# Performance work log

Measured on AMD Instinct MI355X. Metric: run time of the kernel, lower is better.

## Reference

```python
import jax, jax.numpy as jnp
import numpy as np

NUM_HEADS = 8
TOP_M = 128


def setup_inputs() -> dict:
    key = jax.random.key(0)
    ks = jax.random.split(key, 4)
    B, N, C = 2, 4096, 512
    x = jax.random.normal(ks[0], (B, N, C), dtype=jnp.float32)
    # nn.Linear-style params (stored as [in, out] for x @ W)
    qkv_w = jax.random.normal(ks[1], (C, 3 * C), dtype=jnp.float32) * (C ** -0.5)
    qkv_b = jnp.zeros((3 * C,), dtype=jnp.float32)
    proj_w = jax.random.normal(ks[2], (C, C), dtype=jnp.float32) * (C ** -0.5)
    proj_b = jnp.zeros((C,), dtype=jnp.float32)
    return {"x": x, "qkv_w": qkv_w, "qkv_b": qkv_b, "proj_w": proj_w, "proj_b": proj_b}


def reference(x, qkv_w, qkv_b, proj_w, proj_b):
    B, N, C = x.shape
    H = NUM_HEADS
    hd = C // H
    scale = hd ** -0.5

    qkv = x @ qkv_w + qkv_b                       # [B, N, 3C]
    qkv = qkv.reshape(B, N, 3, H, hd).transpose(2, 0, 3, 1, 4)  # [3, B, H, N, hd]
    q, k, v = qkv[0], qkv[1], qkv[2]

    attn = jnp.einsum("bhnd,bhmd->bhnm", q, k) * scale  # [B, H, N, N]

    if TOP_M < N:
        _, topk_idx = jax.lax.top_k(attn, TOP_M)         # [B, H, N, m]
        keep = jnp.put_along_axis(
            jnp.zeros(attn.shape, dtype=bool), topk_idx, True, axis=-1, inplace=False
        )
        attn = jnp.where(keep, attn, -jnp.inf)

    p = jax.nn.softmax(attn, axis=-1)                    # dropout is identity (p=0)
    out = jnp.einsum("bhnm,bhmd->bhnd", p, v)            # [B, H, N, hd]
    out = out.transpose(0, 2, 1, 3).reshape(B, N, C)
    return out @ proj_w + proj_b
```

## Files before the change

kernel.cpp:

```cpp
#include <hip/hip_runtime.h>
#include <cstdint>
#include <cstddef>


typedef float f32x4 __attribute__((ext_vector_type(4)));
typedef __bf16 bf16x8 __attribute__((ext_vector_type(8)));
typedef __bf16 bf16x4 __attribute__((ext_vector_type(4)));

#define MFMA16(a, b, c) __builtin_amdgcn_mfma_f32_16x16x32_bf16((a), (b), (c), 0, 0, 0)

static __device__ __forceinline__ void async_ld16(const void* g, void* l) {
  __builtin_amdgcn_global_load_lds(
      (const __attribute__((address_space(1))) unsigned int*)g,
      (__attribute__((address_space(3))) unsigned int*)l, 16, 0, 0);
}

static __device__ __forceinline__ float bf16raw_to_f32(unsigned r) {
  return __uint_as_float(r << 16);
}

__global__ void k_split(const float* __restrict__ src, __bf16* __restrict__ dh,
                        __bf16* __restrict__ dl, int n) {
  const int i = (blockIdx.x * 256 + threadIdx.x) * 4;
  if (i >= n) return;
  const float4 v = *(const float4*)(src + i);
  bf16x4 h, l;
  h[0] = (__bf16)v.x; l[0] = (__bf16)(v.x - (float)h[0]);
  h[1] = (__bf16)v.y; l[1] = (__bf16)(v.y - (float)h[1]);
  h[2] = (__bf16)v.z; l[2] = (__bf16)(v.z - (float)h[2]);
  h[3] = (__bf16)v.w; l[3] = (__bf16)(v.w - (float)h[3]);
  *(bf16x4*)(dh + i) = h;
  *(bf16x4*)(dl + i) = l;
}

__global__ void k_splitT(const float* __restrict__ src, __bf16* __restrict__ dh,
                         __bf16* __restrict__ dl, int N) {
  const int idx = blockIdx.x * 256 + threadIdx.x;
  const int k = idx & 511;
  const int n = idx >> 9;
  if (n >= N) return;
  const float v = src[(size_t)k * N + n];
  const __bf16 hi = (__bf16)v;
  dh[idx] = hi;
  dl[idx] = (__bf16)(v - (float)hi);
}

template <int MODE>
__global__ __launch_bounds__(256, 2) void k_gemm(
    const __bf16* __restrict__ Agh, const __bf16* __restrict__ Agl,
    const __bf16* __restrict__ Bgh, const __bf16* __restrict__ Bgl,
    const float* __restrict__ bias, float* __restrict__ Cout,
    __bf16* __restrict__ qh, __bf16* __restrict__ ql,
    __bf16* __restrict__ kf,
    __bf16* __restrict__ vv, int N, int K) {
  __shared__ __bf16 sAh[4096], sAl[4096], sBh[4096], sBl[4096];

  const int tid = threadIdx.x;
  const int lane = tid & 63;
  const int wave = tid >> 6;
  const int wm = wave >> 1, wn = wave & 1;
  const int row0 = blockIdx.x * 128;
  const int col0 = blockIdx.y * 128;
  const int m15 = lane & 15, q4 = lane >> 4;

  f32x4 acc[4][4] = {};

  for (int k0 = 0; k0 < K; k0 += 32) {
    __syncthreads();
#pragma unroll
    for (int c = 0; c < 2; ++c) {
      const int s = c * 4 + wave;
      const int gr = s * 16 + m15;
      const int gk = k0 + q4 * 8;
      const size_t aoff = (size_t)(row0 + gr) * K + gk;
      const size_t boff = (size_t)(col0 + gr) * K + gk;
      const int lb = s * 512;
      async_ld16(Agh + aoff, sAh + lb);
      async_ld16(Agl + aoff, sAl + lb);
      async_ld16(Bgh + boff, sBh + lb);
      async_ld16(Bgl + boff, sBl + lb);
    }
    __syncthreads();

    bf16x8 afh[4], afl[4];
#pragma unroll
    for (int mt = 0; mt < 4; ++mt) {
      const int o = (wm * 4 + mt) * 512 + lane * 8;
      afh[mt] = *(const bf16x8*)(sAh + o);
      afl[mt] = *(const bf16x8*)(sAl + o);
    }
#pragma unroll
    for (int nt = 0; nt < 4; ++nt) {
      const int o = (wn * 4 + nt) * 512 + lane * 8;
      const bf16x8 bfh = *(const bf16x8*)(sBh + o);
      const bf16x8 bfl = *(const bf16x8*)(sBl + o);
#pragma unroll
      for (int mt = 0; mt < 4; ++mt) {
        acc[mt][nt] = MFMA16(afh[mt], bfh, acc[mt][nt]);
        acc[mt][nt] = MFMA16(afh[mt], bfl, acc[mt][nt]);
        acc[mt][nt] = MFMA16(afl[mt], bfh, acc[mt][nt]);
      }
    }
  }

#pragma unroll
  for (int mt = 0; mt < 4; ++mt) {
#pragma unroll
    for (int nt = 0; nt < 4; ++nt) {
      const int col = col0 + wn * 64 + nt * 16 + m15;
      const float bcol = bias[col];
#pragma unroll
      for (int r = 0; r < 4; ++r) {
        const int row = row0 + wm * 64 + mt * 16 + q4 * 4 + r;
        const float val = acc[mt][nt][r] + bcol;
        if (MODE == 1) {
          Cout[(size_t)row * N + col] = val;
        } else {
          const int t = col >> 9;
          const int cc = col & 511;
          const int h = cc >> 6, d = cc & 63;
          const int b = row >> 12, n = row & 4095;
          const int bh2 = b * 8 + h;
          if (t == 2) {
            vv[((size_t)bh2 * 4096 + n) * 64 + d] = (__bf16)val;
          } else if (t == 0) {
            const float sv = val * 0.125f;
            const __bf16 hi = (__bf16)sv;
            const size_t o = ((size_t)bh2 * 4096 + n) * 64 + d;
            qh[o] = hi;
            ql[o] = (__bf16)(sv - (float)hi);
          } else {
            const int tt = n >> 4, m = n & 15;
            const int half = d >> 5, q4e = (d & 31) >> 3, e = d & 7;
            const size_t o = ((size_t)(bh2 * 256 + tt) * 4 + half) * 512 +
                             (q4e * 16 + m) * 8 + e;
            const __bf16 hi = (__bf16)val;
            kf[o] = hi;
            kf[o + 1024] = (__bf16)(val - (float)hi);
          }
        }
      }
    }
  }
}

#define CAP 432
#define NBINS 128
__global__ __launch_bounds__(1024, 8) void k_attn(
    const __bf16* __restrict__ qh, const __bf16* __restrict__ ql,
    const __bf16* __restrict__ kf,
    const __bf16* __restrict__ vv, __bf16* __restrict__ ah,
    __bf16* __restrict__ al) {
  __shared__ unsigned int cand[32][CAP];
  __shared__ unsigned int hist[16][NBINS];
  __shared__ unsigned int blist[16][48];
  __shared__ float rsum[32], rsum2[32], t0s[32], invq[32], dqs[32], mrefs[32];
  __shared__ unsigned int ccnt[32];
  __shared__ unsigned int bcnt[16];

  const int tid = threadIdx.x;
  const int lane = tid & 63;
  const int wave = tid >> 6;
  const int m15 = lane & 15, q4 = lane >> 4;
  const int rt = wave & 1;
  const int cr = wave >> 1;
  const int cbase = cr * 512;

  const int L = blockIdx.x;
  const int s = L >> 3;
  const int bh = (L & 7) * 2 + (s >> 7);
  const int row0 = (s & 127) * 32;
  const size_t base = (size_t)bh * 4096 * 64;

  if (tid < 32) { rsum[tid] = 0.f; rsum2[tid] = 0.f; ccnt[tid] = 0; }
  __syncthreads();

  bf16x8 qfh[2], qfl[2];
  {
    const size_t qo = base + (size_t)(row0 + rt * 16 + m15) * 64 + q4 * 8;
    qfh[0] = *(const bf16x8*)(qh + qo);
    qfl[0] = *(const bf16x8*)(ql + qo);
    qfh[1] = *(const bf16x8*)(qh + qo + 32);
    qfl[1] = *(const bf16x8*)(ql + qo + 32);
  }
  const __bf16* kt_base = kf + ((size_t)(bh * 256 + cr * 32) * 4) * 512;
  const int l8 = lane * 8;

  {
    float s1[4] = {0.f, 0.f, 0.f, 0.f}, s2[4] = {0.f, 0.f, 0.f, 0.f};
    for (int j = 0; j < 8; ++j) {
      const __bf16* kt = kt_base + (size_t)(j * 4) * 2048;
      const bf16x8 ch0 = *(const bf16x8*)(kt + l8);
      const bf16x8 ch1 = *(const bf16x8*)(kt + 512 + l8);
      const bf16x8 cl0 = *(const bf16x8*)(kt + 1024 + l8);
      const bf16x8 cl1 = *(const bf16x8*)(kt + 1536 + l8);
      f32x4 a = {0.f, 0.f, 0.f, 0.f};
      a = MFMA16(qfh[0], ch0, a);
      a = MFMA16(qfh[1], ch1, a);
      a = MFMA16(qfh[0], cl0, a);
      a = MFMA16(qfh[1], cl1, a);
      a = MFMA16(qfl[0], ch0, a);
      a = MFMA16(qfl[1], ch1, a);
#pragma unroll
      for (int r = 0; r < 4; ++r) { s1[r] += a[r]; s2[r] += a[r] * a[r]; }
    }
#pragma unroll
    for (int o = 1; o < 16; o <<= 1)
#pragma unroll
      for (int r = 0; r < 4; ++r) {
        s1[r] += __shfl_xor(s1[r], o);
        s2[r] += __shfl_xor(s2[r], o);
      }
    if (m15 == 0) {
#pragma unroll
      for (int r = 0; r < 4; ++r) {
        atomicAdd(&rsum[rt * 16 + q4 * 4 + r], s1[r]);
        atomicAdd(&rsum2[rt * 16 + q4 * 4 + r], s2[r]);
      }
    }
  }
  __syncthreads();
  if (tid < 32) {
    const float mu = rsum[tid] * (1.f / 1024.f);
    float var = rsum2[tid] * (1.f / 1024.f) - mu * mu;
    const float sd = sqrtf(fmaxf(var, 1e-12f));
    t0s[tid] = mu + 1.45f * sd;
    invq[tid] = 1048575.0f / (8.0f * sd);
    dqs[tid]  = (8.0f * sd) * (1.0f / 1048576.0f);
    mrefs[tid] = mu + 5.0f * sd;
  }
  __syncthreads();

  float t0r[4], ivr[4];
#pragma unroll
  for (int r = 0; r < 4; ++r) {
    t0r[r] = t0s[rt * 16 + q4 * 4 + r];
    ivr[r] = invq[rt * 16 + q4 * 4 + r];
  }

  for (int t = 0; t < 32; ++t) {
    const __bf16* kt = kt_base + (size_t)t * 2048;
    const bf16x8 ch0 = *(const bf16x8*)(kt + l8);
    const bf16x8 ch1 = *(const bf16x8*)(kt + 512 + l8);
    const bf16x8 cl0 = *(const bf16x8*)(kt + 1024 + l8);
    const bf16x8 cl1 = *(const bf16x8*)(kt + 1536 + l8);
    f32x4 a = {0.f, 0.f, 0.f, 0.f};
    a = MFMA16(qfh[0], ch0, a);
    a = MFMA16(qfh[1], ch1, a);
    a = MFMA16(qfh[0], cl0, a);
    a = MFMA16(qfh[1], cl1, a);
    a = MFMA16(qfl[0], ch0, a);
    a = MFMA16(qfl[1], ch1, a);
    const unsigned col = (unsigned)(cbase + t * 16 + m15);
#pragma unroll
    for (int r = 0; r < 4; ++r) {
      const float sc = a[r];
      if (sc > t0r[r]) {
        const int row = rt * 16 + q4 * 4 + r;
        int qv = (int)((sc - t0r[r]) * ivr[r]);
        qv = qv > 0xFFFFF ? 0xFFFFF : qv;
        const unsigned e = ((unsigned)qv << 12) | col;
        const unsigned idx = atomicAdd(&ccnt[row], 1u);
        if (idx < CAP) cand[row][idx] = e;
      }
    }
  }
  __syncthreads();

  const unsigned long long bel = (1ull << lane) - 1ull;
  for (int j = 0; j < 2; ++j) {
    const int row = wave * 2 + j;
    const unsigned cnt = min(ccnt[row], (unsigned)CAP);
    const float t0 = t0s[row], dq = dqs[row], mref = mrefs[row];

    hist[wave][lane] = 0;
    hist[wave][lane + 64] = 0;
    if (lane == 0) bcnt[wave] = 0;
    for (unsigned i = lane; i < cnt; i += 64)
      atomicAdd(&hist[wave][cand[row][i] >> 25], 1u);

    const unsigned h0 = hist[wave][2 * lane];
    const unsigned h1 = hist[wave][2 * lane + 1];
    unsigned S = h0 + h1;
    for (int o = 1; o < 64; o <<= 1) {
      const unsigned tmp = __shfl_down(S, o);
      if (lane + o < 64) S += tmp;
    }
    unsigned Snext = __shfl_down(S, 1);
    if (lane == 63) Snext = 0;
    const bool owner = (S >= 128u) && (Snext < 128u);
    const unsigned long long msk = __ballot(owner);
    unsigned thrE = 0;
    if (msk != 0ull) {
      const int ol = __ffsll((unsigned long long)msk) - 1;
      int Bv = 0;
      unsigned rv = 128;
      if (owner) {
        if (Snext + h1 >= 128u) { Bv = 2 * lane + 1; rv = 128u - Snext; }
        else { Bv = 2 * lane; rv = 128u - (Snext + h1); }
      }
      const int B = __shfl(Bv, ol);
      const unsigned rneed = (unsigned)__shfl((int)rv, ol);
      for (unsigned i = lane; i < cnt; i += 64) {
        const unsigned e = cand[row][i];
        if ((int)(e >> 25) == B) {
          const unsigned u = atomicAdd(&bcnt[wave], 1u);
          if (u < 48) blist[wave][u] = e;
        }
      }
      const unsigned ml = min(bcnt[wave], 48u);
      const unsigned mye = (lane < (int)ml) ? blist[wave][lane] : 0u;
      unsigned rlt = 0;
      for (unsigned jj = 0; jj < ml; ++jj)
        rlt += (blist[wave][jj] > mye) ? 1u : 0u;
      const bool hit = (lane < (int)ml) && (rlt == rneed - 1u);
      const unsigned long long hm = __ballot(hit);
      if (hm != 0ull) thrE = __shfl(mye, __ffsll((unsigned long long)hm) - 1);
    }

    unsigned outc = 0;
    float zpart = 0.f;
    for (unsigned c = 0; c * 64 < cnt; ++c) {
      const unsigned i = c * 64 + lane;
      bool sl = false;
      unsigned e = 0;
      if (i < cnt) { e = cand[row][i]; sl = (e >= thrE); }
      const unsigned long long mb = __ballot(sl);
      if (sl) {
        const unsigned pos = outc + (unsigned)__popcll(mb & bel);
        const float scr = t0 + (float)(e >> 12) * dq;
        const float p = __expf(scr - mref);
        zpart += p;
        cand[row][pos] = (__float_as_uint(p) & 0xFFFFF000u) | (e & 0xFFFu);
      }
      outc += (unsigned)__popcll(mb);
    }
#pragma unroll
    for (int o = 1; o < 64; o <<= 1) zpart += __shfl_xor(zpart, o);
    const int n = (int)outc;

    {
      const char* vb2 = (const char*)(vv + base) + lane * 2;
      float o8[8] = {0.f, 0.f, 0.f, 0.f, 0.f, 0.f, 0.f, 0.f};
      int i = 0;
      for (; i + 8 <= n; i += 8) {
        unsigned e0 = cand[row][i + 0], e1 = cand[row][i + 1];
        unsigned e2 = cand[row][i + 2], e3 = cand[row][i + 3];
        unsigned e4 = cand[row][i + 4], e5 = cand[row][i + 5];
        unsigned e6 = cand[row][i + 6], e7 = cand[row][i + 7];
        const unsigned r0 = *(const unsigned short*)(vb2 + (size_t)(e0 & 0xFFFu) * 128);
        const unsigned r1 = *(const unsigned short*)(vb2 + (size_t)(e1 & 0xFFFu) * 128);
        const unsigned r2 = *(const unsigned short*)(vb2 + (size_t)(e2 & 0xFFFu) * 128);
        const unsigned r3 = *(const unsigned short*)(vb2 + (size_t)(e3 & 0xFFFu) * 128);
        const unsigned r4 = *(const unsigned short*)(vb2 + (size_t)(e4 & 0xFFFu) * 128);
        const unsigned r5 = *(const unsigned short*)(vb2 + (size_t)(e5 & 0xFFFu) * 128);
        const unsigned r6 = *(const unsigned short*)(vb2 + (size_t)(e6 & 0xFFFu) * 128);
        const unsigned r7 = *(const unsigned short*)(vb2 + (size_t)(e7 & 0xFFFu) * 128);
        o8[0] += __uint_as_float(e0 & 0xFFFFF000u) * bf16raw_to_f32(r0);
        o8[1] += __uint_as_float(e1 & 0xFFFFF000u) * bf16raw_to_f32(r1);
        o8[2] += __uint_as_float(e2 & 0xFFFFF000u) * bf16raw_to_f32(r2);
        o8[3] += __uint_as_float(e3 & 0xFFFFF000u) * bf16raw_to_f32(r3);
        o8[4] += __uint_as_float(e4 & 0xFFFFF000u) * bf16raw_to_f32(r4);
        o8[5] += __uint_as_float(e5 & 0xFFFFF000u) * bf16raw_to_f32(r5);
        o8[6] += __uint_as_float(e6 & 0xFFFFF000u) * bf16raw_to_f32(r6);
        o8[7] += __uint_as_float(e7 & 0xFFFFF000u) * bf16raw_to_f32(r7);
      }
      for (; i < n; ++i) {
        const unsigned e = cand[row][i];
        const unsigned rr = *(const unsigned short*)(vb2 + (size_t)(e & 0xFFFu) * 128);
        o8[0] += __uint_as_float(e & 0xFFFFF000u) * bf16raw_to_f32(rr);
      }
      const float tot = ((o8[0] + o8[1]) + (o8[2] + o8[3])) +
                        ((o8[4] + o8[5]) + (o8[6] + o8[7]));
      const float outv = tot / fmaxf(zpart, 1e-30f);
      const int b = bh >> 3, hh2 = bh & 7;
      const size_t off =
          ((size_t)(b * 4096 + row0 + row)) * 512 + hh2 * 64 + lane;
      const __bf16 hi = (__bf16)outv;
      ah[off] = hi;
      al[off] = (__bf16)(outv - (float)hi);
    }
  }
}

extern "C" void kernel_launch(void* const* d_in, const int* in_sizes, int n_in,
                              void* d_out, int out_size, void* d_ws, size_t ws_size,
                              hipStream_t stream) {
  const float* x      = (const float*)d_in[0];
  const float* qkv_w  = (const float*)d_in[1];
  const float* qkv_b  = (const float*)d_in[2];
  const float* proj_w = (const float*)d_in[3];
  const float* proj_b = (const float*)d_in[4];
  float* out = (float*)d_out;

  char* w = (char*)d_ws;
  __bf16* xh  = (__bf16*)(w + 0);
  __bf16* xl  = (__bf16*)(w + 8388608);
  __bf16* wqh = (__bf16*)(w + 16777216);
  __bf16* wql = (__bf16*)(w + 18350080);
  __bf16* wph = (__bf16*)(w + 19922944);
  __bf16* wpl = (__bf16*)(w + 20447232);
  __bf16* Qh  = (__bf16*)(w + 20971520);
  __bf16* Ql  = (__bf16*)(w + 29360128);
  __bf16* Kf  = (__bf16*)(w + 37748736);
  __bf16* Vv  = (__bf16*)(w + 54525952);

  k_split<<<4096, 256, 0, stream>>>(x, xh, xl, 4194304);
  k_splitT<<<(1536 * 512) / 256, 256, 0, stream>>>(qkv_w, wqh, wql, 1536);
  k_splitT<<<(512 * 512) / 256, 256, 0, stream>>>(proj_w, wph, wpl, 512);

  {
    dim3 g(64, 12);
    k_gemm<0><<<g, 256, 0, stream>>>(xh, xl, wqh, wql, qkv_b, nullptr,
                                     Qh, Ql, Kf, Vv, 1536, 512);
  }

  k_attn<<<2048, 1024, 0, stream>>>(Qh, Ql, Kf, Vv, xh, xl);

  {
    dim3 g(64, 4);
    k_gemm<1><<<g, 256, 0, stream>>>(xh, xl, wph, wpl, proj_b, out,
                                     nullptr, nullptr, nullptr, nullptr,
                                     512, 512);
  }
}
```

Baseline: 466.7 us.

## Vectorize sparse PV gather, store raw float deltas, trim stats MFMAs

The P·V gather now has each lane load 16-byte vectors of V rows, with 8 candidates processed per step across lane groups, and reduces with shuffles. Each lane previously issued a 2-byte load per candidate. Candidate encoding changes from a quantized score to the truncated float bits of (score − threshold), with histogram bins taken from exponent/mantissa bits relative to a per-row base. This removes the quantization arithmetic. The mean/std sampling pass drops the low-part correction MFMAs, so the statistics become slightly less precise.

```diff
diff --git a/kernel.cpp b/kernel.cpp
--- a/kernel.cpp
+++ b/kernel.cpp
@@ -13,10 +13,6 @@
   __builtin_amdgcn_global_load_lds(
       (const __attribute__((address_space(1))) unsigned int*)g,
       (__attribute__((address_space(3))) unsigned int*)l, 16, 0, 0);
-}
-
-static __device__ __forceinline__ float bf16raw_to_f32(unsigned r) {
-  return __uint_as_float(r << 16);
 }
 
 __global__ void k_split(const float* __restrict__ src, __bf16* __restrict__ dh,
@@ -154,7 +150,8 @@
   __shared__ unsigned int cand[32][CAP];
   __shared__ unsigned int hist[16][NBINS];
   __shared__ unsigned int blist[16][48];
-  __shared__ float rsum[32], rsum2[32], t0s[32], invq[32], dqs[32], mrefs[32];
+  __shared__ float rsum[32], rsum2[32], t0s[32], mrefs[32];
+  __shared__ int cbs[32];
   __shared__ unsigned int ccnt[32];
   __shared__ unsigned int bcnt[16];
 
@@ -192,15 +189,9 @@
       const __bf16* kt = kt_base + (size_t)(j * 4) * 2048;
       const bf16x8 ch0 = *(const bf16x8*)(kt + l8);
       const bf16x8 ch1 = *(const bf16x8*)(kt + 512 + l8);
-      const bf16x8 cl0 = *(const bf16x8*)(kt + 1024 + l8);
-      const bf16x8 cl1 = *(const bf16x8*)(kt + 1536 + l8);
       f32x4 a = {0.f, 0.f, 0.f, 0.f};
       a = MFMA16(qfh[0], ch0, a);
       a = MFMA16(qfh[1], ch1, a);
-      a = MFMA16(qfh[0], cl0, a);
-      a = MFMA16(qfh[1], cl1, a);
-      a = MFMA16(qfl[0], ch0, a);
-      a = MFMA16(qfl[1], ch1, a);
 #pragma unroll
       for (int r = 0; r < 4; ++r) { s1[r] += a[r]; s2[r] += a[r] * a[r]; }
     }
@@ -225,18 +216,14 @@
     float var = rsum2[tid] * (1.f / 1024.f) - mu * mu;
     const float sd = sqrtf(fmaxf(var, 1e-12f));
     t0s[tid] = mu + 1.45f * sd;
-    invq[tid] = 1048575.0f / (8.0f * sd);
-    dqs[tid]  = (8.0f * sd) * (1.0f / 1048576.0f);
+    cbs[tid] = (int)(__float_as_uint(8.0f * sd) >> 21) - 127;
     mrefs[tid] = mu + 5.0f * sd;
   }
   __syncthreads();
 
-  float t0r[4], ivr[4];
-#pragma unroll
-  for (int r = 0; r < 4; ++r) {
-    t0r[r] = t0s[rt * 16 + q4 * 4 + r];
-    ivr[r] = invq[rt * 16 + q4 * 4 + r];
-  }
+  float t0r[4];
+#pragma unroll
+  for (int r = 0; r < 4; ++r) t0r[r] = t0s[rt * 16 + q4 * 4 + r];
 
   for (int t = 0; t < 32; ++t) {
     const __bf16* kt = kt_base + (size_t)t * 2048;
@@ -254,12 +241,10 @@
     const unsigned col = (unsigned)(cbase + t * 16 + m15);
 #pragma unroll
     for (int r = 0; r < 4; ++r) {
-      const float sc = a[r];
-      if (sc > t0r[r]) {
+      const float d = a[r] - t0r[r];
+      if (d > 0.f) {
         const int row = rt * 16 + q4 * 4 + r;
-        int qv = (int)((sc - t0r[r]) * ivr[r]);
-        qv = qv > 0xFFFFF ? 0xFFFFF : qv;
-        const unsigned e = ((unsigned)qv << 12) | col;
+        const unsigned e = (__float_as_uint(d) & 0xFFFFF000u) | col;
         const unsigned idx = atomicAdd(&ccnt[row], 1u);
         if (idx < CAP) cand[row][idx] = e;
       }
@@ -271,13 +256,18 @@
   for (int j = 0; j < 2; ++j) {
     const int row = wave * 2 + j;
     const unsigned cnt = min(ccnt[row], (unsigned)CAP);
-    const float t0 = t0s[row], dq = dqs[row], mref = mrefs[row];
+    const float t0 = t0s[row], mref = mrefs[row];
+    const float mt0 = mref - t0;
+    const int cb = cbs[row];
 
     hist[wave][lane] = 0;
     hist[wave][lane + 64] = 0;
     if (lane == 0) bcnt[wave] = 0;
-    for (unsigned i = lane; i < cnt; i += 64)
-      atomicAdd(&hist[wave][cand[row][i] >> 25], 1u);
+    for (unsigned i = lane; i < cnt; i += 64) {
+      int bb = (int)(cand[row][i] >> 21) - cb;
+      bb = bb < 0 ? 0 : (bb > 127 ? 127 : bb);
+      atomicAdd(&hist[wave][bb], 1u);
+    }
 
     const unsigned h0 = hist[wave][2 * lane];
     const unsigned h1 = hist[wave][2 * lane + 1];
@@ -303,7 +293,9 @@
       const unsigned rneed = (unsigned)__shfl((int)rv, ol);
       for (unsigned i = lane; i < cnt; i += 64) {
         const unsigned e = cand[row][i];
-        if ((int)(e >> 25) == B) {
+        int bb = (int)(e >> 21) - cb;
+        bb = bb < 0 ? 0 : (bb > 127 ? 127 : bb);
+        if (bb == B) {
           const unsigned u = atomicAdd(&bcnt[wave], 1u);
           if (u < 48) blist[wave][u] = e;
         }
@@ -328,8 +320,8 @@
       const unsigned long long mb = __ballot(sl);
       if (sl) {
         const unsigned pos = outc + (unsigned)__popcll(mb & bel);
-        const float scr = t0 + (float)(e >> 12) * dq;
-        const float p = __expf(scr - mref);
+        const float dsc = __uint_as_float(e & 0xFFFFF000u);
+        const float p = __expf(dsc - mt0);
         zpart += p;
         cand[row][pos] = (__float_as_uint(p) & 0xFFFFF000u) | (e & 0xFFFu);
       }
@@ -340,45 +332,51 @@
     const int n = (int)outc;
 
     {
-      const char* vb2 = (const char*)(vv + base) + lane * 2;
-      float o8[8] = {0.f, 0.f, 0.f, 0.f, 0.f, 0.f, 0.f, 0.f};
-      int i = 0;
-      for (; i + 8 <= n; i += 8) {
-        unsigned e0 = cand[row][i + 0], e1 = cand[row][i + 1];
-        unsigned e2 = cand[row][i + 2], e3 = cand[row][i + 3];
-        unsigned e4 = cand[row][i + 4], e5 = cand[row][i + 5];
-        unsigned e6 = cand[row][i + 6], e7 = cand[row][i + 7];
-        const unsigned r0 = *(const unsigned short*)(vb2 + (size_t)(e0 & 0xFFFu) * 128);
-        const unsigned r1 = *(const unsigned short*)(vb2 + (size_t)(e1 & 0xFFFu) * 128);
-        const unsigned r2 = *(const unsigned short*)(vb2 + (size_t)(e2 & 0xFFFu) * 128);
-        const unsigned r3 = *(const unsigned short*)(vb2 + (size_t)(e3 & 0xFFFu) * 128);
-        const unsigned r4 = *(const unsigned short*)(vb2 + (size_t)(e4 & 0xFFFu) * 128);
-        const unsigned r5 = *(const unsigned short*)(vb2 + (size_t)(e5 & 0xFFFu) * 128);
-        const unsigned r6 = *(const unsigned short*)(vb2 + (size_t)(e6 & 0xFFFu) * 128);
-        const unsigned r7 = *(const unsigned short*)(vb2 + (size_t)(e7 & 0xFFFu) * 128);
-        o8[0] += __uint_as_float(e0 & 0xFFFFF000u) * bf16raw_to_f32(r0);
-        o8[1] += __uint_as_float(e1 & 0xFFFFF000u) * bf16raw_to_f32(r1);
-        o8[2] += __uint_as_float(e2 & 0xFFFFF000u) * bf16raw_to_f32(r2);
-        o8[3] += __uint_as_float(e3 & 0xFFFFF000u) * bf16raw_to_f32(r3);
-        o8[4] += __uint_as_float(e4 & 0xFFFFF000u) * bf16raw_to_f32(r4);
-        o8[5] += __uint_as_float(e5 & 0xFFFFF000u) * bf16raw_to_f32(r5);
-        o8[6] += __uint_as_float(e6 & 0xFFFFF000u) * bf16raw_to_f32(r6);
-        o8[7] += __uint_as_float(e7 & 0xFFFFF000u) * bf16raw_to_f32(r7);
-      }
-      for (; i < n; ++i) {
-        const unsigned e = cand[row][i];
-        const unsigned rr = *(const unsigned short*)(vb2 + (size_t)(e & 0xFFFu) * 128);
-        o8[0] += __uint_as_float(e & 0xFFFFF000u) * bf16raw_to_f32(rr);
-      }
-      const float tot = ((o8[0] + o8[1]) + (o8[2] + o8[3])) +
-                        ((o8[4] + o8[5]) + (o8[6] + o8[7]));
-      const float outv = tot / fmaxf(zpart, 1e-30f);
-      const int b = bh >> 3, hh2 = bh & 7;
-      const size_t off =
-          ((size_t)(b * 4096 + row0 + row)) * 512 + hh2 * 64 + lane;
-      const __bf16 hi = (__bf16)outv;
-      ah[off] = hi;
-      al[off] = (__bf16)(outv - (float)hi);
+      const int g8 = lane >> 3, s8 = lane & 7;
+      const char* vL = (const char*)(vv + base) + s8 * 16;
+      float a0 = 0.f, a1 = 0.f, a2 = 0.f, a3 = 0.f;
+      float a4 = 0.f, a5 = 0.f, a6 = 0.f, a7 = 0.f;
+      for (int i = 0; i < n; i += 8) {
+        const int ei = i + g8;
+        const int en = ei < n ? ei : 0;
+        const unsigned e = cand[row][en];
+        float p = __uint_as_float(e & 0xFFFFF000u);
+        if (ei >= n) p = 0.f;
+        const uint4 vd = *(const uint4*)(vL + (size_t)(e & 0xFFFu) * 128);
+        a0 += p * __uint_as_float(vd.x << 16);
+        a1 += p * __uint_as_float(vd.x & 0xFFFF0000u);
+        a2 += p * __uint_as_float(vd.y << 16);
+        a3 += p * __uint_as_float(vd.y & 0xFFFF0000u);
+        a4 += p * __uint_as_float(vd.z << 16);
+        a5 += p * __uint_as_float(vd.z & 0xFFFF0000u);
+        a6 += p * __uint_as_float(vd.w << 16);
+        a7 += p * __uint_as_float(vd.w & 0xFFFF0000u);
+      }
+#pragma unroll
+      for (int o = 8; o < 64; o <<= 1) {
+        a0 += __shfl_xor(a0, o); a1 += __shfl_xor(a1, o);
+        a2 += __shfl_xor(a2, o); a3 += __shfl_xor(a3, o);
+        a4 += __shfl_xor(a4, o); a5 += __shfl_xor(a5, o);
+        a6 += __shfl_xor(a6, o); a7 += __shfl_xor(a7, o);
+      }
+      const float zinv = 1.f / fmaxf(zpart, 1e-30f);
+      if (g8 == 0) {
+        bf16x8 oh, ol;
+        float ov;
+        ov = a0 * zinv; oh[0] = (__bf16)ov; ol[0] = (__bf16)(ov - (float)oh[0]);
+        ov = a1 * zinv; oh[1] = (__bf16)ov; ol[1] = (__bf16)(ov - (float)oh[1]);
+        ov = a2 * zinv; oh[2] = (__bf16)ov; ol[2] = (__bf16)(ov - (float)oh[2]);
+        ov = a3 * zinv; oh[3] = (__bf16)ov; ol[3] = (__bf16)(ov - (float)oh[3]);
+        ov = a4 * zinv; oh[4] = (__bf16)ov; ol[4] = (__bf16)(ov - (float)oh[4]);
+        ov = a5 * zinv; oh[5] = (__bf16)ov; ol[5] = (__bf16)(ov - (float)oh[5]);
+        ov = a6 * zinv; oh[6] = (__bf16)ov; ol[6] = (__bf16)(ov - (float)oh[6]);
+        ov = a7 * zinv; oh[7] = (__bf16)ov; ol[7] = (__bf16)(ov - (float)oh[7]);
+        const int b = bh >> 3, hh2 = bh & 7;
+        const size_t off =
+            ((size_t)(b * 4096 + row0 + row)) * 512 + hh2 * 64 + s8 * 8;
+        *(bf16x8*)(ah + off) = oh;
+        *(bf16x8*)(al + off) = ol;
+      }
     }
   }
 }
```

Result: faster. 401.2 us (-14.0%).
